# Performance work log

Measured on AMD Instinct MI355X. Metric: run time of the kernel, lower is better.

Reference implementation:

```python
import jax, jax.numpy as jnp
import numpy as np

JACCARD_THRESH = 0.5
NEG_POS = 3
VAR0, VAR1 = 0.1, 0.2
MAX_POS = 256  # static cap on gathered positives for the metric-learning terms


def point_form(boxes):
    # (cx,cy,w,h) -> (xmin,ymin,xmax,ymax)
    return jnp.concatenate([boxes[:, :2] - boxes[:, 2:] / 2,
                            boxes[:, :2] + boxes[:, 2:] / 2], axis=1)


def jaccard(a, b):
    # a: [O,4], b: [D,4] point form
    lt = jnp.maximum(a[:, None, :2], b[None, :, :2])
    rb = jnp.minimum(a[:, None, 2:], b[None, :, 2:])
    wh = jnp.clip(rb - lt, 0.0)
    inter = wh[..., 0] * wh[..., 1]
    area_a = (a[:, 2] - a[:, 0]) * (a[:, 3] - a[:, 1])
    area_b = (b[:, 2] - b[:, 0]) * (b[:, 3] - b[:, 1])
    return inter / (area_a[:, None] + area_b[None, :] - inter)


def encode(matched, priors):
    g_cxcy = ((matched[:, :2] + matched[:, 2:]) / 2 - priors[:, :2]) / (VAR0 * priors[:, 2:])
    g_wh = jnp.log((matched[:, 2:] - matched[:, :2]) / priors[:, 2:]) / VAR1
    return jnp.concatenate([g_cxcy, g_wh], axis=1)


def match_one(truths, labels, poses, priors):
    # standard SSD match (per image)
    ov = jaccard(truths, point_form(priors))          # [O, D]
    best_prior_idx = jnp.argmax(ov, axis=1)           # [O]
    best_truth_ov = jnp.max(ov, axis=0)               # [D]
    best_truth_idx = jnp.argmax(ov, axis=0)           # [D]
    best_truth_ov = best_truth_ov.at[best_prior_idx].set(2.0)
    best_truth_idx = best_truth_idx.at[best_prior_idx].set(jnp.arange(truths.shape[0]))
    matches = truths[best_truth_idx]                  # [D,4]
    conf = labels[best_truth_idx] + 1                 # background=0
    conf = jnp.where(best_truth_ov < JACCARD_THRESH, 0, conf)
    return encode(matches, priors), conf.astype(jnp.int32), poses[best_truth_idx]


def multibox_loss(loc_data, conf_data, line_data, pose_data, dbox_list, targets):
    B, D, C = conf_data.shape
    truths = targets[:, :, 0:4]
    labels = targets[:, :, 4].astype(jnp.int32)
    poses = targets[:, :, 5:8]
    loc_t, conf_t, pose_t = jax.vmap(match_one, in_axes=(0, 0, 0, None))(
        truths, labels, poses, dbox_list)

    pos = conf_t > 0                                  # [B,D]
    posf = pos.astype(loc_data.dtype)

    # smooth-L1 loc loss over positives (sum reduction)
    d = loc_data - loc_t
    sl1 = jnp.where(jnp.abs(d) < 1.0, 0.5 * d * d, jnp.abs(d) - 0.5)
    loss_l = jnp.sum(sl1 * posf[..., None])

    # pose squared-error over positives
    loss_p = jnp.sum((pose_data - pose_t) ** 2 * posf[..., None])

    # per-anchor cross entropy + hard-negative mining (double-argsort rank trick)
    logp = jax.nn.log_softmax(conf_data, axis=-1)
    ce = -jnp.take_along_axis(logp, conf_t[..., None], axis=-1)[..., 0]  # [B,D]
    ce_mined = jnp.where(pos, 0.0, ce)
    loss_idx = jnp.argsort(-ce_mined, axis=1)
    idx_rank = jnp.argsort(loss_idx, axis=1)
    num_pos = jnp.sum(pos.astype(jnp.int32), axis=1, keepdims=True)
    num_neg = jnp.minimum(num_pos * NEG_POS, D)
    neg = idx_rank < num_neg
    loss_c = jnp.sum(ce * (pos | neg).astype(ce.dtype))

    N = jnp.maximum(jnp.sum(posf), 1.0)
    loss_l = loss_l / N
    loss_c = loss_c / N
    loss_p = loss_p / N

    # ---- metric-learning block on gathered positives (static cap) ----
    pos_flat = pos.reshape(-1)
    order = jnp.argsort(jnp.where(pos_flat, 0, 1))[:MAX_POS]  # stable: row-major positives first
    valid = pos_flat[order]                                   # [K]
    emb = line_data.reshape(-1, line_data.shape[-1])[order]   # [K,32] raw embeddings
    lab = conf_t.reshape(-1)[order]                           # [K]
    qp = pose_t.reshape(-1, 3)[order]                         # [K,3]

    # PairMarginMiner / TripletMarginLoss use L2-normalized LpDistance by default
    nemb = emb / jnp.maximum(jnp.linalg.norm(emb, axis=1, keepdims=True), 1e-12)
    sq = jnp.sum((nemb[:, None, :] - nemb[None, :, :]) ** 2, axis=-1)
    dist = jnp.sqrt(jnp.maximum(sq, 1e-12))                   # [K,K]

    K = emb.shape[0]
    eye = jnp.eye(K, dtype=bool)
    vpair = valid[:, None] & valid[None, :] & ~eye
    same = lab[:, None] == lab[None, :]
    pos_pair = vpair & same & (dist > 0.2)   # mined hard positive pairs
    neg_pair = vpair & ~same & (dist < 0.8)  # mined hard negative pairs
    n_pp = jnp.sum(pos_pair)
    n_np = jnp.sum(neg_pair)

    # pairs -> triplets sharing the anchor; TripletMarginLoss(margin=0.2), AvgNonZero reducer
    trip_mask = pos_pair[:, :, None] & neg_pair[:, None, :]           # [K,K,K]
    trip_loss = jax.nn.relu(dist[:, :, None] - dist[:, None, :] + 0.2)
    nz = trip_mask & (trip_loss > 0)
    loss_t = jnp.sum(jnp.where(nz, trip_loss, 0.0)) / jnp.maximum(jnp.sum(nz), 1)

    # Ldesk over mined positive pairs: raw-embedding sq-dist vs pose sq-dist consistency
    e_sq = jnp.sum((emb[:, None, :] - emb[None, :, :]) ** 2, axis=-1)
    q_sq = jnp.sum((qp[:, None, :] - qp[None, :, :]) ** 2, axis=-1)
    desk_sum = jnp.sum(jnp.where(pos_pair, (e_sq - q_sq) ** 2, 0.0))
    npp = jnp.maximum(n_pp, 1).astype(loc_data.dtype)
    Ldesk = desk_sum / npp + loss_t / jnp.maximum(n_pp + n_np, 1)
    Ldesk = Ldesk / npp / 32.0

    return loss_l, loss_c, loss_p, Ldesk, loss_t


def setup_inputs():
    key = jax.random.key(0)
    ks = jax.random.split(key, 10)
    B, D, C, L, O = 32, 8732, 21, 32, 8
    loc_data = jax.random.normal(ks[0], (B, D, 4)) * 0.1
    conf_data = jax.random.normal(ks[1], (B, D, C))
    line_data = jax.random.normal(ks[2], (B, D, L))
    pose_data = jax.random.normal(ks[3], (B, D, 3))
    # default boxes (cx,cy,w,h) in (0,1)
    cxcy = jax.random.uniform(ks[4], (D, 2), minval=0.05, maxval=0.95)
    wh = jax.random.uniform(ks[5], (D, 2), minval=0.05, maxval=0.4)
    dbox_list = jnp.concatenate([cxcy, wh], axis=1)
    # targets: [xmin,ymin,xmax,ymax,label,pose(3),unused]
    mins = jax.random.uniform(ks[6], (B, O, 2), minval=0.0, maxval=0.6)
    sizes = jax.random.uniform(ks[7], (B, O, 2), minval=0.1, maxval=0.4)
    boxes = jnp.concatenate([mins, mins + sizes], axis=-1)
    labs = jax.random.randint(ks[8], (B, O, 1), 0, C - 1).astype(jnp.float32)
    pz = jax.random.normal(ks[9], (B, O, 3))
    targets = jnp.concatenate([boxes, labs, pz, jnp.zeros((B, O, 1))], axis=-1)
    return dict(loc_data=loc_data, conf_data=conf_data, line_data=line_data,
                pose_data=pose_data, dbox_list=dbox_list, targets=targets)


def reference(loc_data, conf_data, line_data, pose_data, dbox_list, targets):
    return multibox_loss(loc_data, conf_data, line_data, pose_data, dbox_list, targets)
```

## Files before the change

kernel.cpp:

```cpp
#include <hip/hip_runtime.h>
#include <cstdint>

#define B 32
#define D 8732
#define C 21
#define L 32
#define O 8
#define NS 8
#define SLICE 1092
#define NT 1024

struct Ws {
  const float *loc, *conf, *line, *pose, *dbox, *targets;
  float* out;
  unsigned long long* bp;
  int* cnt;
  int* posSlice;
  float* sce;
  double *gLossL, *gLossP, *gCeP;
  double *gCeNeg;
  double *gDesk, *gNpp, *gNnp, *gTripS, *gTripC;
  int* gPc;
  float *emb, *nemb, *qp; int* lab;
};

__device__ inline double waveSumD(double v) {
  #pragma unroll
  for (int s = 32; s > 0; s >>= 1) v += __shfl_down(v, s, 64);
  return v;
}

__device__ inline float iou_one(float tx1, float ty1, float tx2, float ty2, float ta,
                                float px1, float py1, float px2, float py2, float areaB) {
  float lx = fmaxf(tx1, px1), ly = fmaxf(ty1, py1);
  float rx = fminf(tx2, px2), ry = fminf(ty2, py2);
  float iw = fmaxf(rx - lx, 0.f), ih = fmaxf(ry - ly, 0.f);
  float inter = iw * ih;
  return inter / (ta + areaB - inter);
}

__global__ __launch_bounds__(256) void k_bp(Ws p) {
  __shared__ float tb[O][4], ta[O];
  __shared__ unsigned long long wm[4][O];
  int g = blockIdx.x, tid = threadIdx.x;
  int lane = tid & 63, wav = tid >> 6;
  int b = g >> 3, s = g & 7;
  int dBeg = s * SLICE;
  int dEnd = dBeg + SLICE; if (dEnd > D) dEnd = D;
  if (tid < O) {
    const float* tr = p.targets + ((size_t)b * O + tid) * 9;
    tb[tid][0] = tr[0]; tb[tid][1] = tr[1]; tb[tid][2] = tr[2]; tb[tid][3] = tr[3];
    ta[tid] = (tr[2] - tr[0]) * (tr[3] - tr[1]);
  }
  __syncthreads();
  unsigned long long key[O];
  #pragma unroll
  for (int t = 0; t < O; t++) key[t] = 0ull;
  for (int d = dBeg + tid; d < dEnd; d += 256) {
    float4 db = *(const float4*)(p.dbox + (size_t)d * 4);
    float px1 = db.x - 0.5f*db.z, py1 = db.y - 0.5f*db.w;
    float px2 = db.x + 0.5f*db.z, py2 = db.y + 0.5f*db.w;
    float areaB = db.z * db.w;
    #pragma unroll
    for (int t = 0; t < O; t++) {
      float iou = iou_one(tb[t][0], tb[t][1], tb[t][2], tb[t][3], ta[t],
                          px1, py1, px2, py2, areaB);
      unsigned long long kk = ((unsigned long long)__float_as_uint(iou) << 32)
                            | (unsigned long long)(0xFFFFFFFFu - (unsigned)d);
      if (kk > key[t]) key[t] = kk;
    }
  }
  #pragma unroll
  for (int t = 0; t < O; t++) {
    unsigned long long k = key[t];
    #pragma unroll
    for (int sft = 32; sft > 0; sft >>= 1) {
      unsigned long long o = __shfl_down(k, sft, 64);
      if (o > k) k = o;
    }
    if (lane == 0) wm[wav][t] = k;
  }
  __syncthreads();
  if (tid < O) {
    unsigned long long k = wm[0][tid];
    #pragma unroll
    for (int w = 1; w < 4; w++) if (wm[w][tid] > k) k = wm[w][tid];
    atomicMax(&p.bp[b * O + tid], k);
  }
}

__global__ __launch_bounds__(NT) void k_slice(Ws p) {
  __shared__ float tb[O][4], ta[O], tl[O], tp_[O][3];
  __shared__ int bpd[O];
  __shared__ int plist[256];
  __shared__ int wcnt[16], wbase[16];
  __shared__ double wred[16][3];
  __shared__ int run;
  int g = blockIdx.x, tid = threadIdx.x;
  int lane = tid & 63, wav = tid >> 6;
  const unsigned long long lt = (lane == 0) ? 0ull : (~0ull >> (64 - lane));
  int b = g >> 3, s = g & 7;
  int dBeg = s * SLICE;
  int dEnd = dBeg + SLICE; if (dEnd > D) dEnd = D;

  if (tid < O) {
    const float* tr = p.targets + ((size_t)b * O + tid) * 9;
    tb[tid][0] = tr[0]; tb[tid][1] = tr[1]; tb[tid][2] = tr[2]; tb[tid][3] = tr[3];
    ta[tid] = (tr[2] - tr[0]) * (tr[3] - tr[1]);
    tl[tid] = tr[4];
    tp_[tid][0] = tr[5]; tp_[tid][1] = tr[6]; tp_[tid][2] = tr[7];
  }
  if (tid >= 64 && tid < 64 + O) {
    unsigned long long k = p.bp[b * O + (tid - 64)];
    bpd[tid - 64] = (int)(0xFFFFFFFFu - (unsigned)(k & 0xFFFFFFFFull));
  }
  if (tid == 0) run = 0;
  __syncthreads();

  double ll = 0, lp = 0, cp = 0;
  for (int d0 = dBeg; d0 < dEnd; d0 += NT) {
    int d = d0 + tid;
    bool act = d < dEnd;
    int cls = 0, bi = 0;
    if (act) {
      float4 db = *(const float4*)(p.dbox + (size_t)d * 4);
      float px1 = db.x - 0.5f*db.z, py1 = db.y - 0.5f*db.w;
      float px2 = db.x + 0.5f*db.z, py2 = db.y + 0.5f*db.w;
      float areaB = db.z * db.w;
      float bv = -1.0f;
      #pragma unroll
      for (int t = 0; t < O; t++) {
        float iou = iou_one(tb[t][0], tb[t][1], tb[t][2], tb[t][3], ta[t],
                            px1, py1, px2, py2, areaB);
        if (iou > bv) { bv = iou; bi = t; }
      }
      #pragma unroll
      for (int t = O - 1; t >= 0; t--)
        if (bpd[t] == d) { bi = t; bv = 2.0f; break; }
      cls = (bv < 0.5f) ? 0 : ((int)tl[bi] + 1);
      const float* cb = p.conf + ((size_t)b * D + d) * C;
      float x[C];
      #pragma unroll
      for (int c = 0; c < C; c++) x[c] = cb[c];
      float m = x[0];
      #pragma unroll
      for (int c = 1; c < C; c++) m = fmaxf(m, x[c]);
      float sm = 0.f;
      #pragma unroll
      for (int c = 0; c < C; c++) sm += __expf(x[c] - m);
      float xc = x[0];
      #pragma unroll
      for (int c = 1; c < C; c++) xc = (cls == c) ? x[c] : xc;
      float ce = m + __logf(sm) - xc;
      size_t bd = (size_t)b * D + d;
      if (cls > 0) {
        cp += ce;
        p.sce[bd] = 0.f;
        float g0 = ((tb[bi][0] + tb[bi][2]) * 0.5f - db.x) / (0.1f * db.z);
        float g1 = ((tb[bi][1] + tb[bi][3]) * 0.5f - db.y) / (0.1f * db.w);
        float g2 = logf((tb[bi][2] - tb[bi][0]) / db.z) / 0.2f;
        float g3 = logf((tb[bi][3] - tb[bi][1]) / db.w) / 0.2f;
        float4 lo = *(const float4*)(p.loc + bd * 4);
        float dv, a;
        dv = lo.x - g0; a = fabsf(dv); ll += (double)((a < 1.f) ? 0.5f*dv*dv : a - 0.5f);
        dv = lo.y - g1; a = fabsf(dv); ll += (double)((a < 1.f) ? 0.5f*dv*dv : a - 0.5f);
        dv = lo.z - g2; a = fabsf(dv); ll += (double)((a < 1.f) ? 0.5f*dv*dv : a - 0.5f);
        dv = lo.w - g3; a = fabsf(dv); ll += (double)((a < 1.f) ? 0.5f*dv*dv : a - 0.5f);
        const float* po = p.pose + bd * 3;
        #pragma unroll
        for (int q = 0; q < 3; q++) {
          float pd = po[q] - tp_[bi][q];
          lp += (double)pd * (double)pd;
        }
      } else {
        p.sce[bd] = fmaxf(ce, 0.f);
      }
    }
    bool pos = act && (cls > 0);
    unsigned long long mm = __ballot(pos);
    if (lane == 0) wcnt[wav] = __popcll(mm);
    __syncthreads();
    if (tid == 0) {
      int r = run;
      #pragma unroll
      for (int w = 0; w < 16; w++) { wbase[w] = r; r += wcnt[w]; }
      run = r;
    }
    __syncthreads();
    if (pos) {
      int rank = wbase[wav] + __popcll(mm & lt);
      if (rank < 256) plist[rank] = d | (cls << 14) | (bi << 19);
    }
    __syncthreads();
  }
  int tot = run;
  if (tid == 0) p.cnt[g] = tot;
  int stored = (tot < 256) ? tot : 256;
  if (tid < stored) p.posSlice[g * 256 + tid] = plist[tid];
  double a0 = waveSumD(ll), a1 = waveSumD(lp), a2 = waveSumD(cp);
  if (lane == 0) { wred[wav][0] = a0; wred[wav][1] = a1; wred[wav][2] = a2; }
  __syncthreads();
  if (tid == 0) {
    double tll = 0, tlp = 0, tcp = 0;
    #pragma unroll
    for (int w = 0; w < 16; w++) { tll += wred[w][0]; tlp += wred[w][1]; tcp += wred[w][2]; }
    p.gLossL[g] = tll; p.gLossP[g] = tlp; p.gCeP[g] = tcp;
  }
}

__global__ __launch_bounds__(NT) void k_batch(Ws p) {
  __shared__ __align__(16) float sce[D];
  __shared__ int whist[16][256];
  __shared__ int hist[256];
  __shared__ int sc[256];
  __shared__ int p8[NS + 1];
  __shared__ int gbS;
  __shared__ unsigned prefixSh; __shared__ int kkSh;
  __shared__ double wsum[16], wcnt2[16];
  int bb = blockIdx.x, tid = threadIdx.x;
  int lane = tid & 63, wav = tid >> 6;
  if (tid < 256) sc[tid] = p.cnt[tid];
  __syncthreads();
  if (tid == 0) {
    int gb = 0;
    for (int i = 0; i < bb * NS; i++) gb += sc[i];
    gbS = gb;
    int run = 0;
    for (int ss = 0; ss < NS; ss++) { p8[ss] = run; run += sc[bb * NS + ss]; }
    p8[NS] = run;
    if (bb == 0) {
      int totAll = 0;
      for (int i = 0; i < 256; i++) totAll += sc[i];
      *p.gPc = (totAll < 256) ? totAll : 256;
    }
  }
  __syncthreads();
  int gb = gbS, npos = p8[NS];
  int nr = (npos < 256) ? npos : 256;
  if (tid < nr) {
    int r = tid, ss = 0;
    #pragma unroll
    for (int q = 1; q < NS; q++) if (r >= p8[q]) ss = q;
    int idx = r - p8[ss];
    int slot = gb + r;
    if (idx < 256 && slot < 256) {
      int packed = p.posSlice[(bb * NS + ss) * 256 + idx];
      int d   = packed & 0x3FFF;
      int cls = (packed >> 14) & 31;
      int bi  = (packed >> 19) & 7;
      size_t flat = (size_t)bb * D + d;
      const float4* e4 = (const float4*)(p.line + flat * L);
      float4* o4 = (float4*)(p.emb + slot * L);
      float4* n4 = (float4*)(p.nemb + slot * L);
      float4 v[8];
      float nrm2 = 0.f;
      #pragma unroll
      for (int c = 0; c < 8; c++) {
        v[c] = e4[c];
        o4[c] = v[c];
        nrm2 += v[c].x*v[c].x + v[c].y*v[c].y + v[c].z*v[c].z + v[c].w*v[c].w;
      }
      float inv = 1.f / fmaxf(sqrtf(nrm2), 1e-12f);
      #pragma unroll
      for (int c = 0; c < 8; c++) {
        float4 t = v[c];
        t.x *= inv; t.y *= inv; t.z *= inv; t.w *= inv;
        n4[c] = t;
      }
      p.lab[slot] = cls;
      const float* tr = p.targets + ((size_t)bb * O + bi) * 9;
      p.qp[slot * 3 + 0] = tr[5]; p.qp[slot * 3 + 1] = tr[6]; p.qp[slot * 3 + 2] = tr[7];
    }
  }
  const float* ce = p.sce + (size_t)bb * D;
  for (int i = tid; i < D / 4; i += NT)
    ((float4*)sce)[i] = ((const float4*)ce)[i];
  int k = npos * 3; if (k > D) k = D;
  __syncthreads();
  unsigned prefix = 0; int kk = k;
  for (int pass = 0; pass < 4; pass++) {
    int shift = 24 - 8 * pass;
    for (int i = tid; i < 16 * 256; i += NT) ((int*)whist)[i] = 0;
    __syncthreads();
    unsigned himask = (pass == 0) ? 0u : (0xFFFFFFFFu << (shift + 8));
    for (int d = tid; d < D; d += NT) {
      unsigned keyb = __float_as_uint(sce[d]);
      if ((keyb & himask) == (prefix & himask))
        atomicAdd(&whist[wav][(keyb >> shift) & 255], 1);
    }
    __syncthreads();
    if (tid < 256) {
      int h = 0;
      #pragma unroll
      for (int w = 0; w < 16; w++) h += whist[w][tid];
      hist[tid] = h;
    }
    __syncthreads();
    if (tid < 64) {
      int l = tid;
      int h0 = hist[l*4], h1 = hist[l*4+1], h2 = hist[l*4+2], h3 = hist[l*4+3];
      int loc4 = h0 + h1 + h2 + h3;
      int suf = loc4;
      #pragma unroll
      for (int st = 1; st < 64; st <<= 1) {
        int o = __shfl_down(suf, st, 64);
        if (l + st < 64) suf += o;
      }
      int snext = suf - loc4;
      int s3 = snext + h3, s2 = s3 + h2, s1 = s2 + h1, s0 = s1 + h0;
      if (s3 >= kk && snext < kk) { prefixSh = prefix | ((unsigned)(l*4+3) << shift); kkSh = kk - snext; }
      if (s2 >= kk && s3 < kk)    { prefixSh = prefix | ((unsigned)(l*4+2) << shift); kkSh = kk - s3; }
      if (s1 >= kk && s2 < kk)    { prefixSh = prefix | ((unsigned)(l*4+1) << shift); kkSh = kk - s2; }
      if (s0 >= kk && s1 < kk)    { prefixSh = prefix | ((unsigned)(l*4+0) << shift); kkSh = kk - s1; }
    }
    __syncthreads();
    prefix = prefixSh; kk = kkSh;
    __syncthreads();
  }
  float T = __uint_as_float(prefix);
  double sgt = 0.0; int cgt = 0;
  for (int d = tid; d < D; d += NT) {
    float v = sce[d];
    if (__float_as_uint(v) > prefix) { sgt += (double)v; cgt++; }
  }
  double wv = waveSumD(sgt);
  double wc = waveSumD((double)cgt);
  if (lane == 0) { wsum[wav] = wv; wcnt2[wav] = wc; }
  __syncthreads();
  if (tid == 0) {
    double tsg = 0, tcg = 0;
    #pragma unroll
    for (int w = 0; w < 16; w++) { tsg += wsum[w]; tcg += wcnt2[w]; }
    p.gCeNeg[bb] = tsg + ((double)k - tcg) * (double)T;
  }
}

__global__ __launch_bounds__(NT) void k_pt2(Ws p) {
  __shared__ float ei[L], ni[L], qi[3];
  __shared__ float sd[256];
  __shared__ unsigned long long spm[4], snm[4];
  __shared__ double w1[4];
  __shared__ int ppc[4], npc[4];
  __shared__ double wS[16], wC[16];
  __shared__ int liS, pcS;
  int i = blockIdx.x, tid = threadIdx.x;
  int lane = tid & 63, wav = tid >> 6;
  int qq = tid >> 8, j = tid & 255;
  if (tid == 0) { pcS = *p.gPc; liS = p.lab[i]; }
  if (tid < L) { ei[tid] = p.emb[i * L + tid]; ni[tid] = p.nemb[i * L + tid]; }
  if (tid >= L && tid < L + 3) qi[tid - L] = p.qp[i * 3 + (tid - L)];
  __syncthreads();
  int Pc = pcS, li = liS;
  bool vi = (i < Pc);
  bool pp = false, np = false;
  double dsk = 0.0;
  if (qq == 0) {
    bool vj = (j < Pc);
    const float4* nj4 = (const float4*)(p.nemb + j * L);
    const float4* ej4 = (const float4*)(p.emb + j * L);
    float sq = 0.f, esq = 0.f;
    #pragma unroll
    for (int c = 0; c < 8; c++) {
      float4 nn = nj4[c], ee = ej4[c];
      float d0 = ni[c*4+0] - nn.x, d1 = ni[c*4+1] - nn.y;
      float d2 = ni[c*4+2] - nn.z, d3 = ni[c*4+3] - nn.w;
      sq += d0*d0 + d1*d1 + d2*d2 + d3*d3;
      float e0 = ei[c*4+0] - ee.x, e1 = ei[c*4+1] - ee.y;
      float e2 = ei[c*4+2] - ee.z, e3 = ei[c*4+3] - ee.w;
      esq += e0*e0 + e1*e1 + e2*e2 + e3*e3;
    }
    float dd = sqrtf(fmaxf(sq, 1e-12f));
    sd[j] = dd;
    float qsq = 0.f;
    #pragma unroll
    for (int c = 0; c < 3; c++) { float dq = qi[c] - p.qp[j * 3 + c]; qsq += dq * dq; }
    bool vp = vi && vj && (i != j);
    bool same = (li == p.lab[j]);
    pp = vp && same && (dd > 0.2f);
    np = vp && !same && (dd < 0.8f);
    float diff = esq - qsq;
    dsk = pp ? (double)diff * (double)diff : 0.0;
  }
  unsigned long long pb = __ballot(pp), nb = __ballot(np);
  double dw = waveSumD(dsk);
  if (lane == 0 && wav < 4) {
    spm[wav] = pb; snm[wav] = nb; w1[wav] = dw;
    ppc[wav] = (int)__popcll(pb); npc[wav] = (int)__popcll(nb);
  }
  __syncthreads();
  unsigned long long pmw = spm[j >> 6];
  bool pj = (pmw >> (j & 63)) & 1ull;
  float sdj = sd[j];
  double ts = 0.0, tc = 0.0;
  if (pj) {
    for (int it = 0; it < 64; it++) {
      int kx = qq + 4 * it;
      unsigned long long nmw = snm[kx >> 6];
      if ((nmw >> (kx & 63)) & 1ull) {
        float x = sdj - sd[kx] + 0.2f;
        if (x > 0.f) { ts += (double)x; tc += 1.0; }
      }
    }
  }
  ts = waveSumD(ts); tc = waveSumD(tc);
  if (lane == 0) { wS[wav] = ts; wC[wav] = tc; }
  __syncthreads();
  if (tid == 0) {
    double S = 0, Cc = 0;
    #pragma unroll
    for (int w = 0; w < 16; w++) { S += wS[w]; Cc += wC[w]; }
    double dsum = w1[0] + w1[1] + w1[2] + w1[3];
    int pcnt = ppc[0] + ppc[1] + ppc[2] + ppc[3];
    int ncnt = npc[0] + npc[1] + npc[2] + npc[3];
    p.gDesk[i] = dsum; p.gNpp[i] = (double)pcnt; p.gNnp[i] = (double)ncnt;
    p.gTripS[i] = S; p.gTripC[i] = Cc;
  }
}

__global__ __launch_bounds__(256) void k_fin(Ws p) {
  __shared__ double lbuf[4];
  int tid = threadIdx.x;
  auto sumD = [&](const double* a, int n) -> double {
    double v = 0;
    for (int i = tid; i < n; i += 256) v += a[i];
    v = waveSumD(v);
    __syncthreads();
    if ((tid & 63) == 0) lbuf[tid >> 6] = v;
    __syncthreads();
    double r = lbuf[0] + lbuf[1] + lbuf[2] + lbuf[3];
    __syncthreads();
    return r;
  };
  double lossL = sumD(p.gLossL, 256);
  double lossP = sumD(p.gLossP, 256);
  double ceP   = sumD(p.gCeP,   256);
  double ceN   = sumD(p.gCeNeg,  B);
  double desk  = sumD(p.gDesk,  256);
  double npp   = sumD(p.gNpp,   256);
  double nnp   = sumD(p.gNnp,   256);
  double tripS = sumD(p.gTripS, 256);
  double tripC = sumD(p.gTripC, 256);
  double Ntot;
  {
    double v = 0;
    for (int i = tid; i < 256; i += 256) v += (double)p.cnt[i];
    v = waveSumD(v);
    __syncthreads();
    if ((tid & 63) == 0) lbuf[tid >> 6] = v;
    __syncthreads();
    Ntot = lbuf[0] + lbuf[1] + lbuf[2] + lbuf[3];
  }
  if (tid == 0) {
    double N = (Ntot > 0.0) ? Ntot : 1.0;
    p.out[0] = (float)(lossL / N);
    p.out[1] = (float)((ceP + ceN) / N);
    p.out[2] = (float)(lossP / N);
    double cnt = (tripC > 0.0) ? tripC : 1.0;
    double loss_t = tripS / cnt;
    double nppd = (npp > 0.0) ? npp : 1.0;
    double tot = npp + nnp;
    double denom = (tot > 0.0) ? tot : 1.0;
    double Ldesk = desk / nppd + loss_t / denom;
    Ldesk = Ldesk / nppd / 32.0;
    p.out[3] = (float)Ldesk;
    p.out[4] = (float)loss_t;
  }
}

extern "C" void kernel_launch(void* const* d_in, const int* in_sizes, int n_in,
                              void* d_out, int out_size, void* d_ws, size_t ws_size,
                              hipStream_t stream) {
  char* ws = (char*)d_ws;
  size_t off = 0;
  auto alloc = [&](size_t bytes) -> char* {
    char* q = ws + off;
    off += (bytes + 255) & ~(size_t)255;
    return q;
  };
  Ws p;
  p.loc     = (const float*)d_in[0];
  p.conf    = (const float*)d_in[1];
  p.line    = (const float*)d_in[2];
  p.pose    = (const float*)d_in[3];
  p.dbox    = (const float*)d_in[4];
  p.targets = (const float*)d_in[5];
  p.out     = (float*)d_out;
  p.bp       = (unsigned long long*)alloc(B * O * 8);
  p.cnt      = (int*)alloc(256 * 4);
  p.posSlice = (int*)alloc(256 * 256 * 4);
  p.sce      = (float*)alloc((size_t)B * D * 4);
  p.gLossL   = (double*)alloc(256 * 8);
  p.gLossP   = (double*)alloc(256 * 8);
  p.gCeP     = (double*)alloc(256 * 8);
  p.gCeNeg   = (double*)alloc(B * 8);
  p.gDesk    = (double*)alloc(256 * 8);
  p.gNpp     = (double*)alloc(256 * 8);
  p.gNnp     = (double*)alloc(256 * 8);
  p.gTripS   = (double*)alloc(256 * 8);
  p.gTripC   = (double*)alloc(256 * 8);
  p.gPc      = (int*)alloc(256);
  p.emb      = (float*)alloc(256 * L * 4);
  p.nemb     = (float*)alloc(256 * L * 4);
  p.qp       = (float*)alloc(256 * 3 * 4);
  p.lab      = (int*)alloc(256 * 4);

  hipMemsetAsync(p.bp, 0, B * O * 8, stream);
  k_bp   <<<256, 256, 0, stream>>>(p);
  k_slice<<<256, NT, 0, stream>>>(p);
  k_batch<<<B,   NT, 0, stream>>>(p);
  k_pt2  <<<256, NT, 0, stream>>>(p);
  k_fin  <<<1,  256, 0, stream>>>(p);
}
```

Baseline: 155.0 us.

## Stage conf rows through LDS per wave and make best-prior search atomic-free

In k_slice, each wave now copies its 64 rows of class scores into shared memory with coalesced loads. Threads then read their own 21 scores from LDS instead of doing strided global loads, and the max-exp and pick-class loops are fused into one. k_bp now runs one 1024-thread block per image and writes the best-prior key directly. This removes the global atomicMax and the memset of bp. The cost is about 86 KB of LDS in k_slice, which limits occupancy, and only 32 blocks for k_bp, which reduces its parallelism.

```diff
diff --git a/kernel.cpp b/kernel.cpp
--- a/kernel.cpp
+++ b/kernel.cpp
@@ -39,14 +39,11 @@
   return inter / (ta + areaB - inter);
 }
 
-__global__ __launch_bounds__(256) void k_bp(Ws p) {
+__global__ __launch_bounds__(NT) void k_bp(Ws p) {
   __shared__ float tb[O][4], ta[O];
-  __shared__ unsigned long long wm[4][O];
-  int g = blockIdx.x, tid = threadIdx.x;
+  __shared__ unsigned long long wm[16][O];
+  int b = blockIdx.x, tid = threadIdx.x;
   int lane = tid & 63, wav = tid >> 6;
-  int b = g >> 3, s = g & 7;
-  int dBeg = s * SLICE;
-  int dEnd = dBeg + SLICE; if (dEnd > D) dEnd = D;
   if (tid < O) {
     const float* tr = p.targets + ((size_t)b * O + tid) * 9;
     tb[tid][0] = tr[0]; tb[tid][1] = tr[1]; tb[tid][2] = tr[2]; tb[tid][3] = tr[3];
@@ -56,7 +53,7 @@
   unsigned long long key[O];
   #pragma unroll
   for (int t = 0; t < O; t++) key[t] = 0ull;
-  for (int d = dBeg + tid; d < dEnd; d += 256) {
+  for (int d = tid; d < D; d += NT) {
     float4 db = *(const float4*)(p.dbox + (size_t)d * 4);
     float px1 = db.x - 0.5f*db.z, py1 = db.y - 0.5f*db.w;
     float px2 = db.x + 0.5f*db.z, py2 = db.y + 0.5f*db.w;
@@ -84,12 +81,13 @@
   if (tid < O) {
     unsigned long long k = wm[0][tid];
     #pragma unroll
-    for (int w = 1; w < 4; w++) if (wm[w][tid] > k) k = wm[w][tid];
-    atomicMax(&p.bp[b * O + tid], k);
+    for (int w = 1; w < 16; w++) if (wm[w][tid] > k) k = wm[w][tid];
+    p.bp[b * O + tid] = k;
   }
 }
 
 __global__ __launch_bounds__(NT) void k_slice(Ws p) {
+  __shared__ __align__(16) float cwave[16][64 * C + 4];
   __shared__ float tb[O][4], ta[O], tl[O], tp_[O][3];
   __shared__ int bpd[O];
   __shared__ int plist[256];
@@ -121,6 +119,13 @@
   for (int d0 = dBeg; d0 < dEnd; d0 += NT) {
     int d = d0 + tid;
     bool act = d < dEnd;
+    int waveStart = d0 + wav * 64;
+    if (waveStart < dEnd) {
+      const float* cw = p.conf + ((size_t)b * D + waveStart) * C;
+      #pragma unroll
+      for (int r = 0; r < C; r++)
+        cwave[wav][r * 64 + lane] = cw[r * 64 + lane];
+    }
     int cls = 0, bi = 0;
     if (act) {
       float4 db = *(const float4*)(p.dbox + (size_t)d * 4);
@@ -138,19 +143,18 @@
       for (int t = O - 1; t >= 0; t--)
         if (bpd[t] == d) { bi = t; bv = 2.0f; break; }
       cls = (bv < 0.5f) ? 0 : ((int)tl[bi] + 1);
-      const float* cb = p.conf + ((size_t)b * D + d) * C;
-      float x[C];
-      #pragma unroll
-      for (int c = 0; c < C; c++) x[c] = cb[c];
+      const float* x = &cwave[wav][lane * C];
       float m = x[0];
       #pragma unroll
       for (int c = 1; c < C; c++) m = fmaxf(m, x[c]);
       float sm = 0.f;
-      #pragma unroll
-      for (int c = 0; c < C; c++) sm += __expf(x[c] - m);
       float xc = x[0];
       #pragma unroll
-      for (int c = 1; c < C; c++) xc = (cls == c) ? x[c] : xc;
+      for (int c = 0; c < C; c++) {
+        float xv = x[c];
+        sm += __expf(xv - m);
+        xc = (cls == c) ? xv : xc;
+      }
       float ce = m + __logf(sm) - xc;
       size_t bd = (size_t)b * D + d;
       if (cls > 0) {
@@ -504,8 +508,7 @@
   p.qp       = (float*)alloc(256 * 3 * 4);
   p.lab      = (int*)alloc(256 * 4);
 
-  hipMemsetAsync(p.bp, 0, B * O * 8, stream);
-  k_bp   <<<256, 256, 0, stream>>>(p);
+  k_bp   <<<B,   NT, 0, stream>>>(p);
   k_slice<<<256, NT, 0, stream>>>(p);
   k_batch<<<B,   NT, 0, stream>>>(p);
   k_pt2  <<<256, NT, 0, stream>>>(p);
```

New measurement: 167.9 us. 1.08x slower.
